# Performance work log

Measured on AMD Instinct MI355X. Metric: run time of the kernel, lower is better.

## Reference

```python
import jax, jax.numpy as jnp
import numpy as np

D_MODEL = 1024
D_INNER = 2048   # expand=2
D_STATE = 16
D_CONV = 4
DT_RANK = 64     # ceil(d_model/16)
BATCH = 4
SEQLEN = 2048


def setup_inputs() -> dict:
    key = jax.random.key(0)
    ks = jax.random.split(key, 9)
    f = lambda k, shape, s=0.02: jax.random.normal(k, shape, dtype=jnp.float32) * s
    return {
        "x": jax.random.normal(ks[0], (BATCH, SEQLEN, D_MODEL), dtype=jnp.float32),
        "norm_w": jnp.ones((D_MODEL,), jnp.float32),
        "in_proj_w": f(ks[1], (2 * D_INNER, D_MODEL)),
        "conv_w": f(ks[2], (D_INNER, D_CONV), 0.1),
        "conv_b": f(ks[3], (D_INNER,), 0.1),
        "x_proj_w": f(ks[4], (DT_RANK + 2 * D_STATE, D_INNER)),
        "dt_proj_w": f(ks[5], (D_INNER, DT_RANK), 0.1),
        "dt_proj_b": f(ks[6], (D_INNER,), 0.1),
        "A_log": jnp.log(jnp.tile(jnp.arange(1, D_STATE + 1, dtype=jnp.float32), (D_INNER, 1))),
        "D_param": jnp.ones((D_INNER,), jnp.float32),
        "out_proj_w": f(ks[7], (D_MODEL, D_INNER)),
    }


def _rmsnorm(x, w):
    eps = jnp.finfo(jnp.float32).eps
    var = jnp.mean(x * x, axis=-1, keepdims=True)
    return x * jax.lax.rsqrt(var + eps) * w


def _mamba(x_norm, in_proj_w, conv_w, conv_b, x_proj_w,
           dt_proj_w, dt_proj_b, A_log, D_param, out_proj_w):
    B, L, _ = x_norm.shape
    # input projection -> [B, L, 2*D_INNER], split into x and gate z
    xz = jnp.einsum('bld,ed->ble', x_norm, in_proj_w)
    x_in, z = jnp.split(xz, 2, axis=-1)
    # causal depthwise conv1d (kernel D_CONV, left pad D_CONV-1)
    x_c = jax.lax.conv_general_dilated(
        x_in.transpose(0, 2, 1),                 # [B, D_INNER, L]
        conv_w[:, None, :],                      # [D_INNER, 1, D_CONV]
        window_strides=(1,), padding=[(D_CONV - 1, 0)],
        dimension_numbers=('NCH', 'OIH', 'NCH'),
        feature_group_count=D_INNER,
    ) + conv_b[None, :, None]
    u = jax.nn.silu(x_c.transpose(0, 2, 1))      # [B, L, D_INNER]
    # SSM parameters
    x_dbl = jnp.einsum('bld,ed->ble', u, x_proj_w)  # [B, L, DT_RANK+2*D_STATE]
    dt, B_mat, C_mat = jnp.split(x_dbl, [DT_RANK, DT_RANK + D_STATE], axis=-1)
    dt = jax.nn.softplus(jnp.einsum('blr,dr->bld', dt, dt_proj_w) + dt_proj_b)  # [B,L,D_INNER]
    A = -jnp.exp(A_log)                          # [D_INNER, D_STATE]

    # selective scan over time; state h: [B, D_INNER, D_STATE]
    def step(h, inputs):
        dt_t, B_t, C_t, u_t = inputs             # [B,Dn],[B,S],[B,S],[B,Dn]
        dA = jnp.exp(dt_t[:, :, None] * A)       # [B, Dn, S]
        h = dA * h + (dt_t * u_t)[:, :, None] * B_t[:, None, :]
        y_t = jnp.einsum('bds,bs->bd', h, C_t)
        return h, y_t

    h0 = jnp.zeros((B, D_INNER, D_STATE), x_norm.dtype)
    xs = (dt.transpose(1, 0, 2), B_mat.transpose(1, 0, 2),
          C_mat.transpose(1, 0, 2), u.transpose(1, 0, 2))
    _, ys = jax.lax.scan(step, h0, xs)           # [L, B, D_INNER]
    y = ys.transpose(1, 0, 2) + D_param * u
    y = y * jax.nn.silu(z)
    return jnp.einsum('bld,ed->ble', y, out_proj_w)  # [B, L, D_MODEL]


def reference(x, norm_w, in_proj_w, conv_w, conv_b, x_proj_w,
              dt_proj_w, dt_proj_b, A_log, D_param, out_proj_w):
    x_norm = _rmsnorm(x, norm_w)
    out = _mamba(x_norm, in_proj_w, conv_w, conv_b, x_proj_w,
                 dt_proj_w, dt_proj_b, A_log, D_param, out_proj_w)
    return x + out
```

## Files before the change

kernel.cpp:

```cpp
#include <hip/hip_runtime.h>
#include <hip/hip_bf16.h>
#include <math.h>

#define DM 1024
#define DI 2048
#define DS 16
#define DC 4
#define DR 64
#define NB 4
#define SL 2048
#define BL (NB * SL)
#define DXP (DR + 2 * DS)
#define NC 32
#define CL (SL / NC)

typedef __hip_bfloat16 bf16;
typedef __attribute__((ext_vector_type(8))) short short8;
typedef __attribute__((ext_vector_type(4))) float floatx4;
typedef unsigned int u32;

__device__ __forceinline__ float to_f(float v) { return v; }
__device__ __forceinline__ float to_f(bf16 v) { return __bfloat162float(v); }
template <typename T> __device__ __forceinline__ T from_f(float v);
template <> __device__ __forceinline__ float from_f<float>(float v) { return v; }
template <> __device__ __forceinline__ bf16 from_f<bf16>(float v) { return __float2bfloat16(v); }

__device__ __forceinline__ float bfbits2f(unsigned short u) {
  u32 b = ((u32)u) << 16;
  return __builtin_bit_cast(float, b);
}
__device__ __forceinline__ short f2bfbits(float v) {
  bf16 b = __float2bfloat16(v);
  return __builtin_bit_cast(short, b);
}
__device__ __forceinline__ float fsilu(float v) {
  return v * __builtin_amdgcn_rcpf(1.f + __expf(-v));
}

__device__ __forceinline__ void gload16(const ushort* g, ushort* l) {
  __builtin_amdgcn_global_load_lds((const __attribute__((address_space(1))) void*)g,
                                   (__attribute__((address_space(3))) void*)l,
                                   16, 0, 0);
}

__device__ __forceinline__ void vmw4() { asm volatile("s_waitcnt vmcnt(4)" ::: "memory"); }
__device__ __forceinline__ void vmw2() { asm volatile("s_waitcnt vmcnt(2)" ::: "memory"); }
__device__ __forceinline__ void vmw0() { asm volatile("s_waitcnt vmcnt(0)" ::: "memory"); }
__device__ __forceinline__ void barx() {
  asm volatile("" ::: "memory");
  __builtin_amdgcn_s_barrier();
  asm volatile("" ::: "memory");
}

__global__ __launch_bounds__(256) void f2b_k(const float* __restrict__ src,
                                             bf16* __restrict__ dst, int n) {
  int i = blockIdx.x * 256 + threadIdx.x;
  if (i < n) dst[i] = from_f<bf16>(src[i]);
}

__global__ __launch_bounds__(256) void rmsnorm_k(const float* __restrict__ x,
                                                 const float* __restrict__ w,
                                                 bf16* __restrict__ o) {
  int row = blockIdx.x;
  const float* xr = x + (size_t)row * DM;
  float ss = 0.f;
  for (int i = threadIdx.x; i < DM; i += 256) { float v = xr[i]; ss += v * v; }
  for (int off = 32; off > 0; off >>= 1) ss += __shfl_down(ss, off);
  __shared__ float sred[4];
  __shared__ float sscale;
  if ((threadIdx.x & 63) == 0) sred[threadIdx.x >> 6] = ss;
  __syncthreads();
  if (threadIdx.x == 0) {
    float t = sred[0] + sred[1] + sred[2] + sred[3];
    sscale = rsqrtf(t / (float)DM + 1.1920929e-7f);
  }
  __syncthreads();
  float sc = sscale;
  bf16* orow = o + (size_t)row * DM;
  for (int i = threadIdx.x; i < DM; i += 256) orow[i] = from_f<bf16>(xr[i] * sc * w[i]);
}

template <int MODE>
__global__ __launch_bounds__(512, 1) void gemm256(const bf16* __restrict__ A,
                                                  const bf16* __restrict__ W,
                                                  int M, int N, int K,
                                                  bf16* __restrict__ Cx,
                                                  bf16* __restrict__ Cz, int nsplit,
                                                  float* __restrict__ Cf,
                                                  const float* __restrict__ R) {
  __shared__ ushort SH[65536];
  const int tid = threadIdx.x;
  const int lane = tid & 63, wv = tid >> 6;
  const int wr = wv >> 2, wc = wv & 3;
  const int row15 = lane & 15, quad = lane >> 4;

  int ntm = M >> 8, ntn = N >> 8, nwg = ntm * ntn;
  int bid = blockIdx.x;
  int swz = (bid & 7) * (nwg >> 3) + (bid >> 3);
  int bm0 = (swz % ntm) << 8, bn0 = (swz / ntm) << 8;

  const int nt = K >> 6;
  const ushort* Au = (const ushort*)A;
  const ushort* Wu = (const ushort*)W;

  const int w4u = lane ^ (((lane >> 5) & 1) << 1);
  const int Wsw = (((row15 << 6) | (quad << 4)) ^ (((row15 >> 3) & 1) << 5));
  const char* SHb = (const char*)SH;
  const int Abase0 = (wr << 14) + Wsw;
  const int Abase1 = 32768 + (wr << 14) + Wsw;
  const int Bbase0 = 65536 + ((wc >> 1) << 14) + ((wc & 1) << 13) + Wsw;
  const int Bbase1 = Bbase0 + 32768;

  auto stageA = [&](int tt, int half, int buf) {
    const ushort* g = Au + (size_t)(bm0 + half * 128) * K + tt * 64;
    char* lds = (char*)SH + (size_t)(buf * 2 + half) * 16384;
#pragma unroll
    for (int i = 0; i < 2; ++i) {
      int sub = wv + i * 8;
      int r = ((sub >> 1) << 4) | (w4u >> 2);
      int ce = ((sub & 1) << 5) | ((w4u & 3) << 3);
      gload16(g + (size_t)r * K + ce, (ushort*)(lds + sub * 1024));
    }
  };
  auto stageB = [&](int tt, int half, int buf) {
    const ushort* g = Wu + (size_t)(bn0 + half * 128) * K + tt * 64;
    char* lds = (char*)SH + 65536 + (size_t)(buf * 2 + half) * 16384;
#pragma unroll
    for (int i = 0; i < 2; ++i) {
      int sub = wv + i * 8;
      int r = ((sub >> 1) << 4) | (w4u >> 2);
      int ce = ((sub & 1) << 5) | ((w4u & 3) << 3);
      gload16(g + (size_t)r * K + ce, (ushort*)(lds + sub * 1024));
    }
  };

  short8 a_f[4][2], bq[2][2][2];
  floatx4 acc[8][4] = {};

#define LDA_(base, mh) do { _Pragma("unroll") for (int mi = 0; mi < 4; ++mi) \
  { _Pragma("unroll") for (int kk = 0; kk < 2; ++kk) \
    a_f[mi][kk] = *(const short8*)(SHb + (base) + ((((mh)*4 + mi)*2 + kk) << 10)); } } while (0)
#define LDB_(base, nh) do { _Pragma("unroll") for (int ni = 0; ni < 2; ++ni) \
  { _Pragma("unroll") for (int kk = 0; kk < 2; ++kk) \
    bq[nh][ni][kk] = *(const short8*)(SHb + (base) + (((((nh)*2 + ni)*2 + kk)) << 10)); } } while (0)
#define MM_(mh, nh) do { __builtin_amdgcn_s_setprio(1); \
  _Pragma("unroll") for (int mi = 0; mi < 4; ++mi) \
  { _Pragma("unroll") for (int ni = 0; ni < 2; ++ni) \
    { _Pragma("unroll") for (int kk = 0; kk < 2; ++kk) \
      acc[(mh)*4+mi][(nh)*2+ni] = __builtin_amdgcn_mfma_f32_16x16x32_bf16( \
          a_f[mi][kk], bq[nh][ni][kk], acc[(mh)*4+mi][(nh)*2+ni], 0, 0, 0); } } \
  __builtin_amdgcn_s_setprio(0); } while (0)

#define TILE_(t, AB, BB, curbuf, nxtbuf) do { \
  int tp1 = (t) + 1, tp2 = (t) + 2; \
  LDA_(AB, 0); LDB_(BB, 0); \
  if (tp1 < nt) stageA(tp1, 0, nxtbuf); \
  barx(); MM_(0, 0); barx(); \
  LDB_(BB, 1); \
  if (tp1 < nt) stageA(tp1, 1, nxtbuf); \
  barx(); MM_(0, 1); barx(); \
  LDA_(AB, 1); \
  if (tp2 < nt) stageB(tp2, 0, curbuf); \
  barx(); MM_(1, 1); barx(); \
  if (tp2 < nt) stageB(tp2, 1, curbuf); \
  barx(); MM_(1, 0); \
  if (tp2 < nt) vmw4(); else vmw0(); \
  barx(); \
} while (0)

  stageB(0, 0, 0); stageB(0, 1, 0); stageA(0, 0, 0); stageA(0, 1, 0);
  stageB(1, 0, 1); stageB(1, 1, 1);
  vmw4();
  barx();

  for (int t = 0; t < nt; t += 2) {
    TILE_(t, Abase0, Bbase0, 0, 1);
    TILE_(t + 1, Abase1, Bbase1, 1, 0);
  }
#undef TILE_
#undef MM_
#undef LDB_
#undef LDA_

#pragma unroll
  for (int mi8 = 0; mi8 < 8; ++mi8) {
#pragma unroll
    for (int ni4 = 0; ni4 < 4; ++ni4) {
#pragma unroll
      for (int reg = 0; reg < 4; ++reg) {
        int grow = bm0 + wr * 128 + mi8 * 16 + quad * 4 + reg;
        int gcol = bn0 + wc * 64 + ni4 * 16 + row15;
        float v = acc[mi8][ni4][reg];
        if (MODE == 1) {
          if (gcol < nsplit) {
            Cx[(size_t)grow * DI + gcol] = from_f<bf16>(v);
          } else {
            Cz[(size_t)grow * DI + (gcol - nsplit)] = from_f<bf16>(fsilu(v));
          }
        } else {
          size_t o = (size_t)grow * N + gcol;
          Cf[o] = v + R[o];
        }
      }
    }
  }
}

template <int MODE>
__global__ __launch_bounds__(512, 1) void gemm_np(const bf16* __restrict__ A,
                                                  const bf16* __restrict__ W,
                                                  int M, int N, int K,
                                                  bf16* __restrict__ Cx,
                                                  bf16* __restrict__ Cz, int nsplit,
                                                  float* __restrict__ Cf,
                                                  const float* __restrict__ R) {
  __shared__ ushort SH[49152];
  const int tid = threadIdx.x;
  const int lane = tid & 63, wv = tid >> 6;
  const int wr = wv >> 1, wc = wv & 1;
  const int row15 = lane & 15, quad = lane >> 4;

  int ntm = M >> 8, ntn = N >> 7, nwg = ntm * ntn;
  int bid = blockIdx.x;
  int swz = (bid & 7) * (nwg >> 3) + (bid >> 3);
  int bm0 = (swz % ntm) << 8, bn0 = (swz / ntm) << 7;

  const int nt = K >> 6;
  const ushort* Au = (const ushort*)A;
  const ushort* Wu = (const ushort*)W;
  const ushort* Ag = Au + (u32)bm0 * (u32)K;
  const ushort* Bg = Wu + (u32)bn0 * (u32)K;

  const int w4u = lane ^ (((lane >> 5) & 1) << 1);
  const int sub0 = wv, sub1 = wv + 8;
  const int r0 = ((sub0 >> 1) << 4) | (w4u >> 2);
  const int c0 = ((sub0 & 1) << 5) | ((w4u & 3) << 3);
  const int r1 = ((sub1 >> 1) << 4) | (w4u >> 2);
  const int c1 = ((sub1 & 1) << 5) | ((w4u & 3) << 3);
  ushort* shA = (ushort*)SH;
  ushort* shB = (ushort*)SH + 32768;

  auto stage = [&](const ushort* gbase, int rowoff, int tt, ushort* lbase) {
    gload16(gbase + (u32)(rowoff + r0) * (u32)K + (u32)(tt * 64 + c0), lbase + (sub0 << 9));
    gload16(gbase + (u32)(rowoff + r1) * (u32)K + (u32)(tt * 64 + c1), lbase + (sub1 << 9));
  };

  const int Wsw = (((row15 << 6) | (quad << 4)) ^ (((row15 >> 3) & 1) << 5));
  const char* SHb = (const char*)SH;
  const int AB0 = (wr << 13) + Wsw;
  const int AB1 = 32768 + AB0;
  const int BB0 = 65536 + (wc << 13) + Wsw;
  const int BB1 = BB0 + 16384;

  short8 a0[2][2], a1[2][2], bq0A[2][2], bq0B[2][2], bq1[2][2];
  floatx4 acc[4][4] = {};

#define LDA_(dst, base, mh) do { _Pragma("unroll") for (int i_ = 0; i_ < 2; ++i_) \
  { _Pragma("unroll") for (int kk = 0; kk < 2; ++kk) \
    dst[i_][kk] = *(const short8*)(SHb + (base) + ((((mh)*2 + i_)*2 + kk) << 10)); } } while (0)
#define LDB_(dst, base, nh) do { _Pragma("unroll") for (int j_ = 0; j_ < 2; ++j_) \
  { _Pragma("unroll") for (int kk = 0; kk < 2; ++kk) \
    dst[j_][kk] = *(const short8*)(SHb + (base) + ((((nh)*2 + j_)*2 + kk) << 10)); } } while (0)
#define MM_(aset, bset, mh, nh) do { __builtin_amdgcn_s_setprio(1); \
  _Pragma("unroll") for (int i_ = 0; i_ < 2; ++i_) \
  { _Pragma("unroll") for (int j_ = 0; j_ < 2; ++j_) \
    { _Pragma("unroll") for (int kk = 0; kk < 2; ++kk) \
      acc[(mh)*2+i_][(nh)*2+j_] = __builtin_amdgcn_mfma_f32_16x16x32_bf16( \
          aset[i_][kk], bset[j_][kk], acc[(mh)*2+i_][(nh)*2+j_], 0, 0, 0); } } \
  __builtin_amdgcn_s_setprio(0); } while (0)

#define TILE_(t, ABc, BBc, ABn, BBn, BQU, BQF, CURB, NXTB) do { \
  int tp1 = (t) + 1, tp2 = (t) + 2; \
   \
  LDB_(bq1, BBc, 1); \
  if (tp1 < nt) stage(Ag, 0, tp1, shA + (NXTB) * 16384); \
  barx(); MM_(a0, BQU, 0, 0); barx(); \
   \
  LDA_(a1, ABc, 1); \
  if (tp1 < nt) stage(Ag, 128, tp1, shA + (NXTB) * 16384 + 8192); \
  barx(); MM_(a0, bq1, 0, 1); barx(); \
   \
  if (tp2 < nt) stage(Bg, 0, tp2, shB + (CURB) * 8192); \
  barx(); MM_(a1, bq1, 1, 1); \
  if (tp2 < nt) vmw2(); else vmw0(); \
  barx(); \
   \
  if (tp1 < nt) { LDA_(a0, ABn, 0); LDB_(BQF, BBn, 0); } \
  barx(); MM_(a1, BQU, 1, 0); barx(); \
} while (0)

  stage(Bg, 0, 0, shB);
  stage(Ag, 0, 0, shA);
  stage(Ag, 128, 0, shA + 8192);
  if (nt > 1) { stage(Bg, 0, 1, shB + 8192); vmw2(); } else { vmw0(); }
  barx();
  LDA_(a0, AB0, 0);
  LDB_(bq0A, BB0, 0);

  for (int t = 0; t < nt; t += 2) {
    TILE_(t,     AB0, BB0, AB1, BB1, bq0A, bq0B, 0, 1);
    TILE_(t + 1, AB1, BB1, AB0, BB0, bq0B, bq0A, 1, 0);
  }
#undef TILE_
#undef MM_
#undef LDB_
#undef LDA_

#pragma unroll
  for (int mi = 0; mi < 4; ++mi) {
#pragma unroll
    for (int ni = 0; ni < 4; ++ni) {
#pragma unroll
      for (int reg = 0; reg < 4; ++reg) {
        int grow = bm0 + wr * 64 + mi * 16 + quad * 4 + reg;
        int gcol = bn0 + wc * 64 + ni * 16 + row15;
        float v = acc[mi][ni][reg];
        if (MODE == 1) {
          if (gcol < nsplit) {
            Cx[(u32)grow * DI + (u32)gcol] = from_f<bf16>(v);
          } else {
            Cz[(u32)grow * DI + (u32)(gcol - nsplit)] = from_f<bf16>(fsilu(v));
          }
        } else {
          u32 o = (u32)grow * (u32)N + (u32)gcol;
          Cf[o] = v + R[o];
        }
      }
    }
  }
}

#define TM 128
#define TN 128
#define TK 32
#define LDK 40
template <int MODE>
__global__ __launch_bounds__(256) void gemm_mfma(const bf16* __restrict__ A,
                                                 const bf16* __restrict__ W,
                                                 int M, int N, int K,
                                                 bf16* __restrict__ Cx,
                                                 bf16* __restrict__ Cz, int nsplit,
                                                 float* __restrict__ Cf,
                                                 const float* __restrict__ R,
                                                 const float* __restrict__ bias) {
  __shared__ ushort Asm[TM][TK];
  __shared__ ushort Bsm[TN][TK];
  int bm = blockIdx.y * TM, bn = blockIdx.x * TN;
  int tid = threadIdx.x;
  int lane = tid & 63, wave = tid >> 6;
  int wm = (wave & 1) * 64, wn = (wave >> 1) * 64;
  int row15 = lane & 15, quad = lane >> 4;

  int srow = lane >> 2;
  int scol = (lane & 3) * 8;
  int s0 = wave * 2, s1 = wave * 2 + 1;

  const ushort* Au = (const ushort*)A;
  const ushort* Wu = (const ushort*)W;
  const ushort* ag0 = Au + (size_t)(bm + s0 * 16 + srow) * K + scol;
  const ushort* ag1 = Au + (size_t)(bm + s1 * 16 + srow) * K + scol;
  const ushort* bg0 = Wu + (size_t)(bn + s0 * 16 + srow) * K + scol;
  const ushort* bg1 = Wu + (size_t)(bn + s1 * 16 + srow) * K + scol;
  ushort* la0 = &Asm[s0 * 16][0];
  ushort* la1 = &Asm[s1 * 16][0];
  ushort* lb0 = &Bsm[s0 * 16][0];
  ushort* lb1 = &Bsm[s1 * 16][0];

  floatx4 acc[4][4] = {};

  for (int k0 = 0; k0 < K; k0 += TK) {
    gload16(ag0 + k0, la0);
    gload16(ag1 + k0, la1);
    gload16(bg0 + k0, lb0);
    gload16(bg1 + k0, lb1);
    __syncthreads();
    short8 a_f[4], b_f[4];
#pragma unroll
    for (int i = 0; i < 4; ++i)
      a_f[i] = *(const short8*)&Asm[wm + i * 16 + row15][quad * 8];
#pragma unroll
    for (int j = 0; j < 4; ++j)
      b_f[j] = *(const short8*)&Bsm[wn + j * 16 + row15][quad * 8];
#pragma unroll
    for (int i = 0; i < 4; ++i)
#pragma unroll
      for (int j = 0; j < 4; ++j)
        acc[i][j] = __builtin_amdgcn_mfma_f32_16x16x32_bf16(a_f[i], b_f[j], acc[i][j], 0, 0, 0);
    __syncthreads();
  }
#pragma unroll
  for (int mi = 0; mi < 4; ++mi) {
#pragma unroll
    for (int ni = 0; ni < 4; ++ni) {
#pragma unroll
      for (int reg = 0; reg < 4; ++reg) {
        int grow = bm + wm + mi * 16 + quad * 4 + reg;
        int gcol = bn + wn + ni * 16 + row15;
        float v = acc[mi][ni][reg];
        if (MODE == 1) {
          if (gcol < nsplit) {
            Cx[(size_t)grow * DI + gcol] = from_f<bf16>(v);
          } else {
            Cz[(size_t)grow * DI + (gcol - nsplit)] = from_f<bf16>(fsilu(v));
          }
        } else if (MODE == 2) {
          size_t o = (size_t)grow * N + gcol;
          Cf[o] = v + R[o];
        } else {
          float t = v + bias[gcol];
          float sp = (t > 20.f) ? t : __logf(1.f + __expf(t));
          Cx[(size_t)grow * N + gcol] = from_f<bf16>(sp);
        }
      }
    }
  }
}

#define XKS 128
__global__ __launch_bounds__(256) void xproj_k(const bf16* __restrict__ u,
                                               const bf16* __restrict__ w,
                                               float* __restrict__ xdbl) {
  __shared__ ushort Asm[128][LDK];
  __shared__ ushort Bsm[96][LDK];
  int kbase = blockIdx.x * XKS;
  int bm = blockIdx.y * 128;
  int tid = threadIdx.x;
  int lane = tid & 63, wave = tid >> 6;
  int row15 = lane & 15, quad = lane >> 4;
  int srow = tid >> 1, skoff = (tid & 1) * 16;

  floatx4 acc[2][6] = {};
  const ushort* Au = (const ushort*)u;
  const ushort* Wu = (const ushort*)w;
  for (int k0 = kbase; k0 < kbase + XKS; k0 += TK) {
    const ushort* ag = Au + (size_t)(bm + srow) * DI + k0 + skoff;
    *(short8*)&Asm[srow][skoff]     = *(const short8*)ag;
    *(short8*)&Asm[srow][skoff + 8] = *(const short8*)(ag + 8);
    if (tid < 192) {
      const ushort* wg = Wu + (size_t)srow * DI + k0 + skoff;
      *(short8*)&Bsm[srow][skoff]     = *(const short8*)wg;
      *(short8*)&Bsm[srow][skoff + 8] = *(const short8*)(wg + 8);
    }
    __syncthreads();
    short8 a_f[2], b_f[6];
#pragma unroll
    for (int i = 0; i < 2; ++i)
      a_f[i] = *(const short8*)&Asm[wave * 32 + i * 16 + row15][quad * 8];
#pragma unroll
    for (int j = 0; j < 6; ++j)
      b_f[j] = *(const short8*)&Bsm[j * 16 + row15][quad * 8];
#pragma unroll
    for (int i = 0; i < 2; ++i)
#pragma unroll
      for (int j = 0; j < 6; ++j)
        acc[i][j] = __builtin_amdgcn_mfma_f32_16x16x32_bf16(a_f[i], b_f[j], acc[i][j], 0, 0, 0);
    __syncthreads();
  }
#pragma unroll
  for (int mi = 0; mi < 2; ++mi)
#pragma unroll
    for (int nj = 0; nj < 6; ++nj)
#pragma unroll
      for (int reg = 0; reg < 4; ++reg) {
        int grow = bm + wave * 32 + mi * 16 + quad * 4 + reg;
        int gcol = nj * 16 + row15;
        atomicAdd(&xdbl[(size_t)grow * DXP + gcol], acc[mi][nj][reg]);
      }
}

__global__ __launch_bounds__(256) void dtex_k(const float* __restrict__ xdbl,
                                              bf16* __restrict__ dtin) {
  int i = blockIdx.x * 256 + threadIdx.x;
  int r = i >> 6, c = i & 63;
  dtin[i] = from_f<bf16>(xdbl[(size_t)r * DXP + c]);
}

#define TSTRIP 8
__global__ __launch_bounds__(256) void conv_silu_k(const bf16* __restrict__ xin,
                                                   const float* __restrict__ cw,
                                                   const float* __restrict__ cb,
                                                   bf16* __restrict__ u) {
  int blk = blockIdx.x;
  int b = blk >> 8;
  int l0 = (blk & 255) * TSTRIP;
  int c0 = threadIdx.x * 8;

  float4 cw4[8];
  const float4* cwp = (const float4*)cw;
#pragma unroll
  for (int j = 0; j < 8; ++j) cw4[j] = cwp[c0 + j];
  float cbv[8];
  {
    float4 cb0 = *(const float4*)&cb[c0];
    float4 cb1 = *(const float4*)&cb[c0 + 4];
    cbv[0] = cb0.x; cbv[1] = cb0.y; cbv[2] = cb0.z; cbv[3] = cb0.w;
    cbv[4] = cb1.x; cbv[5] = cb1.y; cbv[6] = cb1.z; cbv[7] = cb1.w;
  }

  const ushort* base = (const ushort*)xin + ((size_t)(b * SL + l0) * DI + c0);
  ushort* ubase = (ushort*)u + ((size_t)(b * SL + l0) * DI + c0);

  short8 zz = {};
  short8 w0 = zz, w1 = zz, w2 = zz;
  if (l0 >= 3) {
    w0 = *(const short8*)(base - 3 * DI);
    w1 = *(const short8*)(base - 2 * DI);
    w2 = *(const short8*)(base - 1 * DI);
  }
#pragma unroll
  for (int l = 0; l < TSTRIP; ++l) {
    short8 w3 = *(const short8*)(base + (ptrdiff_t)l * DI);
    short8 outv;
#pragma unroll
    for (int j = 0; j < 8; ++j) {
      float a = cbv[j]
              + bfbits2f((unsigned short)w0[j]) * cw4[j].x
              + bfbits2f((unsigned short)w1[j]) * cw4[j].y
              + bfbits2f((unsigned short)w2[j]) * cw4[j].z
              + bfbits2f((unsigned short)w3[j]) * cw4[j].w;
      outv[j] = f2bfbits(fsilu(a));
    }
    *(short8*)(ubase + (ptrdiff_t)l * DI) = outv;
    w0 = w1; w1 = w2; w2 = w3;
  }
}

__global__ __launch_bounds__(256) void scan_p1(const bf16* __restrict__ dts,
                                               const bf16* __restrict__ u,
                                               const float* __restrict__ xdbl,
                                               const float* __restrict__ A_log,
                                               float* __restrict__ Pbuf,
                                               float* __restrict__ Qbuf) {
  int bid = blockIdx.x;
  int b = bid >> 8;
  int c = (bid >> 3) & (NC - 1);
  int d = (bid & 7) * 256 + threadIdx.x;

  float A[DS], h[DS], P[DS];
#pragma unroll
  for (int s = 0; s < DS; ++s) {
    A[s] = -__expf(A_log[d * DS + s]);
    h[s] = 0.f; P[s] = 1.f;
  }
  size_t bl0 = (size_t)b * SL + c * CL;
  size_t base = bl0 * DI + d;
  size_t xb = bl0 * DXP + DR;
  for (int l = 0; l < CL; ++l) {
    float dtv = to_f(dts[base]);
    float uv = to_f(u[base]);
    float du = dtv * uv;
#pragma unroll
    for (int s = 0; s < DS; ++s) {
      float Bv = xdbl[xb + s];
      float dA = __expf(dtv * A[s]);
      h[s] = dA * h[s] + du * Bv;
      P[s] *= dA;
    }
    base += DI;
    xb += DXP;
  }
  size_t o = ((size_t)(b * NC + c) * DS) * DI + d;
#pragma unroll
  for (int s = 0; s < DS; ++s) {
    Pbuf[o + (size_t)s * DI] = P[s];
    Qbuf[o + (size_t)s * DI] = h[s];
  }
}

__global__ __launch_bounds__(256) void scan_p2(float* __restrict__ Pbuf,
                                               float* __restrict__ Qbuf) {
  int bid = blockIdx.x;
  int b = bid >> 7;
  int s = (bid >> 3) & (DS - 1);
  int d = (bid & 7) * 256 + threadIdx.x;
  float h = 0.f;
  for (int c = 0; c < NC; ++c) {
    size_t idx = ((size_t)((b * NC + c) * DS + s)) * DI + d;
    float Pv = Pbuf[idx];
    float qv = Qbuf[idx];
    Qbuf[idx] = h;
    h = Pv * h + qv;
  }
}

__global__ __launch_bounds__(256) void scan_p3(const bf16* __restrict__ dts,
                                               bf16* __restrict__ u,
                                               const float* __restrict__ xdbl,
                                               const float* __restrict__ A_log,
                                               const float* __restrict__ Dp,
                                               const bf16* __restrict__ g,
                                               const float* __restrict__ Qbuf) {
  int bid = blockIdx.x;
  int b = bid >> 8;
  int c = (bid >> 3) & (NC - 1);
  int d = (bid & 7) * 256 + threadIdx.x;

  float A[DS], h[DS];
  size_t o = ((size_t)(b * NC + c) * DS) * DI + d;
#pragma unroll
  for (int s = 0; s < DS; ++s) {
    A[s] = -__expf(A_log[d * DS + s]);
    h[s] = Qbuf[o + (size_t)s * DI];
  }
  float Dd = Dp[d];
  size_t bl0 = (size_t)b * SL + c * CL;
  size_t base = bl0 * DI + d;
  size_t xb = bl0 * DXP + DR;
  for (int l = 0; l < CL; ++l) {
    float dtv = to_f(dts[base]);
    float uv = to_f(u[base]);
    float gv = to_f(g[base]);
    float du = dtv * uv;
    float p0 = 0.f, p1 = 0.f, p2 = 0.f, p3 = 0.f;
#pragma unroll
    for (int s = 0; s < DS; s += 4) {
      float dA0 = __expf(dtv * A[s + 0]);
      float dA1 = __expf(dtv * A[s + 1]);
      float dA2 = __expf(dtv * A[s + 2]);
      float dA3 = __expf(dtv * A[s + 3]);
      h[s + 0] = dA0 * h[s + 0] + du * xdbl[xb + s + 0];
      h[s + 1] = dA1 * h[s + 1] + du * xdbl[xb + s + 1];
      h[s + 2] = dA2 * h[s + 2] + du * xdbl[xb + s + 2];
      h[s + 3] = dA3 * h[s + 3] + du * xdbl[xb + s + 3];
      p0 += h[s + 0] * xdbl[xb + DS + s + 0];
      p1 += h[s + 1] * xdbl[xb + DS + s + 1];
      p2 += h[s + 2] * xdbl[xb + DS + s + 2];
      p3 += h[s + 3] * xdbl[xb + DS + s + 3];
    }
    float yv = ((p0 + p1) + (p2 + p3)) + Dd * uv;
    u[base] = from_f<bf16>(yv * gv);
    base += DI;
    xb += DXP;
  }
}

extern "C" void kernel_launch(void* const* d_in, const int* in_sizes, int n_in,
                              void* d_out, int out_size, void* d_ws, size_t ws_size,
                              hipStream_t stream) {
  const float* x        = (const float*)d_in[0];
  const float* norm_w   = (const float*)d_in[1];
  const float* in_projw = (const float*)d_in[2];
  const float* conv_w   = (const float*)d_in[3];
  const float* conv_b   = (const float*)d_in[4];
  const float* x_projw  = (const float*)d_in[5];
  const float* dt_projw = (const float*)d_in[6];
  const float* dt_projb = (const float*)d_in[7];
  const float* A_log    = (const float*)d_in[8];
  const float* Dp       = (const float*)d_in[9];
  const float* out_projw= (const float*)d_in[10];
  float* out = (float*)d_out;

  char* wsb = (char*)d_ws;
  bf16* x_buf  = (bf16*)wsb;
  bf16* z_buf  = (bf16*)(wsb + (size_t)BL * DI * 2);
  bf16* u_buf  = (bf16*)(wsb + (size_t)BL * DI * 4);
  char* ovl    = wsb + (size_t)BL * DI * 6;
  bf16* ipw_bf = (bf16*)ovl;
  float* xdbl   = (float*)ovl;
  bf16*  xpw_bf = (bf16*)(ovl + 3145728);
  bf16*  dtw_bf = (bf16*)(ovl + 3538944);
  bf16*  dtin_bf= (bf16*)(ovl + 3801088);
  bf16* xnorm_bf = u_buf;
  bf16* dt_buf   = x_buf;
  bf16* opw_bf   = x_buf;
  float* Pbuf = out;
  float* Qbuf = out + (size_t)NB * NC * DS * DI;

  f2b_k<<<(2 * DI * DM) / 256, 256, 0, stream>>>(in_projw, ipw_bf, 2 * DI * DM);
  rmsnorm_k<<<BL, 256, 0, stream>>>(x, norm_w, xnorm_bf);
  gemm256<1><<<(BL / 256) * (2 * DI / 256), 512, 0, stream>>>(
      xnorm_bf, ipw_bf, BL, 2 * DI, DM, x_buf, z_buf, DI, nullptr, nullptr);
  conv_silu_k<<<NB * (SL / TSTRIP), 256, 0, stream>>>(x_buf, conv_w, conv_b, u_buf);
  hipMemsetAsync(xdbl, 0, (size_t)BL * DXP * sizeof(float), stream);
  f2b_k<<<(DXP * DI + 255) / 256, 256, 0, stream>>>(x_projw, xpw_bf, DXP * DI);
  f2b_k<<<(DI * DR) / 256, 256, 0, stream>>>(dt_projw, dtw_bf, DI * DR);
  xproj_k<<<dim3(DI / XKS, BL / 128), 256, 0, stream>>>(u_buf, xpw_bf, xdbl);
  dtex_k<<<(BL * DR) / 256, 256, 0, stream>>>(xdbl, dtin_bf);
  gemm_mfma<3><<<dim3(DI / TN, BL / TM), 256, 0, stream>>>(
      dtin_bf, dtw_bf, BL, DI, DR, dt_buf, nullptr, 0, nullptr, nullptr, dt_projb);
  scan_p1<<<NB * NC * (DI / 256), 256, 0, stream>>>(dt_buf, u_buf, xdbl, A_log, Pbuf, Qbuf);
  scan_p2<<<NB * DS * (DI / 256), 256, 0, stream>>>(Pbuf, Qbuf);
  scan_p3<<<NB * NC * (DI / 256), 256, 0, stream>>>(dt_buf, u_buf, xdbl, A_log, Dp, z_buf, Qbuf);
  f2b_k<<<(DM * DI) / 256, 256, 0, stream>>>(out_projw, opw_bf, DM * DI);
  gemm_np<2><<<(BL / 256) * (DM / 128), 512, 0, stream>>>(
      u_buf, opw_bf, BL, DM, DI, nullptr, nullptr, 0, out, x);
}
```

Baseline: 466.0 us.

## Replace x_proj atomic split-K with partial buffers and fused reduction

The x_proj GEMM previously split K into 16 chunks and accumulated with float atomicAdd into a zeroed buffer, followed by a separate dt-extraction kernel. Now K is split 8 ways, each split writes its partial sums to its own slice of a scratch buffer (aliasing the output), and a reduction kernel sums the partials, writes xdbl, and emits the bf16 dt input. This removes the memset and atomic contention. The GEMM tile-index mapping is also changed from column-major to row-major ordering in the two large GEMMs, which alters L2 reuse of tiles.

```diff
diff --git a/kernel.cpp b/kernel.cpp
--- a/kernel.cpp
+++ b/kernel.cpp
@@ -13,6 +13,7 @@
 #define DXP (DR + 2 * DS)
 #define NC 32
 #define CL (SL / NC)
+#define XNS 8
 
 typedef __hip_bfloat16 bf16;
 typedef __attribute__((ext_vector_type(8))) short short8;
@@ -97,7 +98,7 @@
   int ntm = M >> 8, ntn = N >> 8, nwg = ntm * ntn;
   int bid = blockIdx.x;
   int swz = (bid & 7) * (nwg >> 3) + (bid >> 3);
-  int bm0 = (swz % ntm) << 8, bn0 = (swz / ntm) << 8;
+  int bm0 = (swz / ntn) << 8, bn0 = (swz % ntn) << 8;
 
   const int nt = K >> 6;
   const ushort* Au = (const ushort*)A;
@@ -223,7 +224,7 @@
   int ntm = M >> 8, ntn = N >> 7, nwg = ntm * ntn;
   int bid = blockIdx.x;
   int swz = (bid & 7) * (nwg >> 3) + (bid >> 3);
-  int bm0 = (swz % ntm) << 8, bn0 = (swz / ntm) << 7;
+  int bm0 = (swz / ntn) << 8, bn0 = (swz % ntn) << 7;
 
   const int nt = K >> 6;
   const ushort* Au = (const ushort*)A;
@@ -416,13 +417,12 @@
   }
 }
 
-#define XKS 128
 __global__ __launch_bounds__(256) void xproj_k(const bf16* __restrict__ u,
                                                const bf16* __restrict__ w,
-                                               float* __restrict__ xdbl) {
+                                               float* __restrict__ Ppart) {
   __shared__ ushort Asm[128][LDK];
   __shared__ ushort Bsm[96][LDK];
-  int kbase = blockIdx.x * XKS;
+  int kbase = blockIdx.x * (DI / XNS);
   int bm = blockIdx.y * 128;
   int tid = threadIdx.x;
   int lane = tid & 63, wave = tid >> 6;
@@ -432,7 +432,7 @@
   floatx4 acc[2][6] = {};
   const ushort* Au = (const ushort*)u;
   const ushort* Wu = (const ushort*)w;
-  for (int k0 = kbase; k0 < kbase + XKS; k0 += TK) {
+  for (int k0 = kbase; k0 < kbase + (DI / XNS); k0 += TK) {
     const ushort* ag = Au + (size_t)(bm + srow) * DI + k0 + skoff;
     *(short8*)&Asm[srow][skoff]     = *(const short8*)ag;
     *(short8*)&Asm[srow][skoff + 8] = *(const short8*)(ag + 8);
@@ -456,6 +456,7 @@
         acc[i][j] = __builtin_amdgcn_mfma_f32_16x16x32_bf16(a_f[i], b_f[j], acc[i][j], 0, 0, 0);
     __syncthreads();
   }
+  float* P = Ppart + (size_t)blockIdx.x * ((size_t)BL * DXP);
 #pragma unroll
   for (int mi = 0; mi < 2; ++mi)
 #pragma unroll
@@ -464,15 +465,20 @@
       for (int reg = 0; reg < 4; ++reg) {
         int grow = bm + wave * 32 + mi * 16 + quad * 4 + reg;
         int gcol = nj * 16 + row15;
-        atomicAdd(&xdbl[(size_t)grow * DXP + gcol], acc[mi][nj][reg]);
+        P[(size_t)grow * DXP + gcol] = acc[mi][nj][reg];
       }
 }
 
-__global__ __launch_bounds__(256) void dtex_k(const float* __restrict__ xdbl,
+__global__ __launch_bounds__(256) void xred_k(const float* __restrict__ Ppart,
+                                              float* __restrict__ xdbl,
                                               bf16* __restrict__ dtin) {
   int i = blockIdx.x * 256 + threadIdx.x;
-  int r = i >> 6, c = i & 63;
-  dtin[i] = from_f<bf16>(xdbl[(size_t)r * DXP + c]);
+  float s = 0.f;
+#pragma unroll
+  for (int p = 0; p < XNS; ++p) s += Ppart[(size_t)p * ((size_t)BL * DXP) + i];
+  xdbl[i] = s;
+  int r = i / DXP, c = i - r * DXP;
+  if (c < DR) dtin[r * DR + c] = from_f<bf16>(s);
 }
 
 #define TSTRIP 8
@@ -663,6 +669,7 @@
   bf16* xnorm_bf = u_buf;
   bf16* dt_buf   = x_buf;
   bf16* opw_bf   = x_buf;
+  float* Ppart = out;
   float* Pbuf = out;
   float* Qbuf = out + (size_t)NB * NC * DS * DI;
 
@@ -671,11 +678,10 @@
   gemm256<1><<<(BL / 256) * (2 * DI / 256), 512, 0, stream>>>(
       xnorm_bf, ipw_bf, BL, 2 * DI, DM, x_buf, z_buf, DI, nullptr, nullptr);
   conv_silu_k<<<NB * (SL / TSTRIP), 256, 0, stream>>>(x_buf, conv_w, conv_b, u_buf);
-  hipMemsetAsync(xdbl, 0, (size_t)BL * DXP * sizeof(float), stream);
   f2b_k<<<(DXP * DI + 255) / 256, 256, 0, stream>>>(x_projw, xpw_bf, DXP * DI);
   f2b_k<<<(DI * DR) / 256, 256, 0, stream>>>(dt_projw, dtw_bf, DI * DR);
-  xproj_k<<<dim3(DI / XKS, BL / 128), 256, 0, stream>>>(u_buf, xpw_bf, xdbl);
-  dtex_k<<<(BL * DR) / 256, 256, 0, stream>>>(xdbl, dtin_bf);
+  xproj_k<<<dim3(XNS, BL / 128), 256, 0, stream>>>(u_buf, xpw_bf, Ppart);
+  xred_k<<<(BL * DXP) / 256, 256, 0, stream>>>(Ppart, xdbl, dtin_bf);
   gemm_mfma<3><<<dim3(DI / TN, BL / TM), 256, 0, stream>>>(
       dtin_bf, dtw_bf, BL, DI, DR, dt_buf, nullptr, 0, nullptr, nullptr, dt_projb);
   scan_p1<<<NB * NC * (DI / 256), 256, 0, stream>>>(dt_buf, u_buf, xdbl, A_log, Pbuf, Qbuf);
```

New measurement: 436.4 us. 1.07x faster.
